# Optimization experiments

Measured on AMD Instinct MI355X. Metric: run time of the kernel, lower is better.

The kernel has to match this reference:

```python
import jax, jax.numpy as jnp
import numpy as np

B, S, D = 8, 1024, 1024   # batch, routed-over rows, feature dim (input_dim)
E = 1024                  # output_dim (== S so gather indices are in range)
K = 2                     # top-k
ALPHA = 0.01


def setup_inputs() -> dict:
    key = jax.random.key(0)
    kx, kw = jax.random.split(key)
    x = jax.random.normal(kx, (B, S, D), dtype=jnp.float32)
    # nn.Linear(input_dim, output_dim, bias=False) weight: [E, D]
    W = jax.random.normal(kw, (E, D), dtype=jnp.float32) / np.sqrt(D).astype(np.float32)
    return {"x": x, "W": W}


def reference(x, W):
    # logits = proj(x): [B, S, E]  (temperature == 1.0 -> no scaling)
    logits = jnp.einsum('bsd,ed->bse', x, W)
    probs = jax.nn.softmax(logits, axis=-1)
    topk_probs, topk_idx = jax.lax.top_k(probs, K)            # [B, S, K]
    # router_selections: gather rows of x along dim 1 -> [B, S, K, D]
    sel = x[jnp.arange(B)[:, None, None], topk_idx]
    # y = sum_k topk_probs * selected rows -> [B, S, D]
    y = jnp.einsum('bsk,bskd->bsd', topk_probs, sel)
    # auxiliary load-balance loss
    router_probs = probs.mean(axis=(0, 1))                    # [E]
    counts = jnp.bincount(topk_idx.reshape(-1), length=E).astype(probs.dtype)
    router_fraction = counts / counts.sum()
    aux_loss = ALPHA * E * jnp.sum(router_probs * router_fraction)
    return y, aux_loss
```

## Files before the change

### kernel.cpp

```cpp
#include <hip/hip_runtime.h>

#define MTOK 8192
#define ED   1024

typedef short s16x8 __attribute__((ext_vector_type(8)));
typedef float f32x4 __attribute__((ext_vector_type(4)));
typedef int   i32x4 __attribute__((ext_vector_type(4)));
typedef unsigned short u16x4 __attribute__((ext_vector_type(4)));

__device__ __forceinline__ unsigned short f2bf(float f) {
    unsigned u = __builtin_bit_cast(unsigned, f);
    u += 0x7fff + ((u >> 16) & 1);
    return (unsigned short)(u >> 16);
}
__device__ __forceinline__ float bf2f(unsigned short h) {
    unsigned u = ((unsigned)h) << 16;
    return __builtin_bit_cast(float, u);
}

__global__ __launch_bounds__(256) void split_bf16_kernel(
        const float* __restrict__ src, unsigned short* __restrict__ hi,
        unsigned short* __restrict__ lo, int n4) {
    int idx = blockIdx.x * 256 + threadIdx.x;
    const int stride = gridDim.x * 256;
    for (; idx < n4; idx += stride) {
        float4 v = ((const float4*)src)[idx];
        u16x4 h, l;
        h[0] = f2bf(v.x); l[0] = f2bf(v.x - bf2f(h[0]));
        h[1] = f2bf(v.y); l[1] = f2bf(v.y - bf2f(h[1]));
        h[2] = f2bf(v.z); l[2] = f2bf(v.z - bf2f(h[2]));
        h[3] = f2bf(v.w); l[3] = f2bf(v.w - bf2f(h[3]));
        ((u16x4*)hi)[idx] = h;
        ((u16x4*)lo)[idx] = l;
    }
}

__device__ __forceinline__ void gload16(const void* g, void* l) {
    __builtin_amdgcn_global_load_lds(
        (const __attribute__((address_space(1))) void*)g,
        (__attribute__((address_space(3))) void*)l, 16, 0, 0);
}

__device__ __forceinline__ int cvtpk(float a, float b) {
    int r;
    asm("v_cvt_pk_bf16_f32 %0, %1, %2" : "=v"(r) : "v"(a), "v"(b));
    return r;
}

__device__ __forceinline__ void cvt_write(void* dstHi, void* dstLo,
                                          const float4 f0, const float4 f1) {
    i32x4 h, l;
    h[0] = cvtpk(f0.x, f0.y); h[1] = cvtpk(f0.z, f0.w);
    h[2] = cvtpk(f1.x, f1.y); h[3] = cvtpk(f1.z, f1.w);
    l[0] = cvtpk(f0.x - __builtin_bit_cast(float, h[0] << 16),
                 f0.y - __builtin_bit_cast(float, h[0] & 0xffff0000));
    l[1] = cvtpk(f0.z - __builtin_bit_cast(float, h[1] << 16),
                 f0.w - __builtin_bit_cast(float, h[1] & 0xffff0000));
    l[2] = cvtpk(f1.x - __builtin_bit_cast(float, h[2] << 16),
                 f1.y - __builtin_bit_cast(float, h[2] & 0xffff0000));
    l[3] = cvtpk(f1.z - __builtin_bit_cast(float, h[3] << 16),
                 f1.w - __builtin_bit_cast(float, h[3] & 0xffff0000));
    *(i32x4*)dstHi = h;
    *(i32x4*)dstLo = l;
}

__global__ __launch_bounds__(256, 2) void gemm_mfma_split_kernel(
        const float* __restrict__ Xf,
        const unsigned short* __restrict__ Whi, const unsigned short* __restrict__ Wlo,
        float* __restrict__ C) {
    __shared__ __align__(16) unsigned char smem[2 * 32768];

    const int bid = blockIdx.x;
    const int xcd = bid & 7;
    const int j   = bid >> 3;
    const int bm  = xcd * 8 + (j >> 3);
    const int bn  = j & 7;

    const int tid  = threadIdx.x;
    const int lane = tid & 63;
    const int wid  = tid >> 6;

    const int srow = lane >> 2;
    const int sg   = (lane & 3) ^ ((lane >> 3) & 3);
    const float* gA = Xf + (size_t)(bm * 128 + wid * 32 + srow) * ED + sg * 8;
    const unsigned short* gB = ((wid < 2) ? Whi : Wlo)
            + (size_t)(bn * 128 + (wid & 1) * 64 + srow) * ED + sg * 8;
    unsigned char* const dB = smem + 16384 + ((wid < 2) ? 0 : 8192) + (wid & 1) * 4096;

    float4 fA0, fA1, fA2, fA3;

#define ALOAD(kk)                                                    \
    fA0 = *(const float4*)(gA + (kk));                               \
    fA1 = *(const float4*)(gA + (kk) + 4);                           \
    fA2 = *(const float4*)(gA + (kk) + 16 * 1024);                   \
    fA3 = *(const float4*)(gA + (kk) + 16 * 1024 + 4);

#define BSTAGE(buf, kk)                                              \
    _Pragma("unroll")                                                \
    for (int c = 0; c < 4; ++c)                                      \
        gload16(gB + (kk) + c * (16 * ED), dB + (buf) * 32768 + c * 1024);

#define AWRITE(buf)                                                              \
    cvt_write(smem + (buf) * 32768 + (2 * wid) * 1024 + lane * 16,               \
              smem + (buf) * 32768 + 8192 + (2 * wid) * 1024 + lane * 16,        \
              fA0, fA1);                                                         \
    cvt_write(smem + (buf) * 32768 + (2 * wid + 1) * 1024 + lane * 16,           \
              smem + (buf) * 32768 + 8192 + (2 * wid + 1) * 1024 + lane * 16,    \
              fA2, fA3);

    const int wm = wid >> 1, wn = wid & 1;
    const int fr = lane & 15, fg = lane >> 4;
    const int pg = fg ^ ((fr >> 1) & 3);
    const int aoff = (wm * 64 + fr) * 32 + pg * 8;
    const int boff = (wn * 64 + fr) * 32 + pg * 8;

    f32x4 acc[4][4] = {};

    ALOAD(0);
    BSTAGE(0, 0);
    AWRITE(0);
    asm volatile("s_waitcnt vmcnt(0) lgkmcnt(0)" ::: "memory");
    __builtin_amdgcn_s_barrier();

    for (int t = 0; t < 32; ++t) {
        const int cur = t & 1;
        if (t < 31) { ALOAD((t + 1) * 32); BSTAGE(cur ^ 1, (t + 1) * 32); }

        const unsigned short* Ah = (const unsigned short*)(smem + cur * 32768);
        const unsigned short* Al = Ah + 4096;
        const unsigned short* Bh = Ah + 8192;
        const unsigned short* Bl = Ah + 12288;

        s16x8 ah[4], al[4], bh[4], bl[4];
#pragma unroll
        for (int i = 0; i < 4; ++i) {
            ah[i] = *(const s16x8*)&Ah[aoff + i * 512];
            al[i] = *(const s16x8*)&Al[aoff + i * 512];
            bh[i] = *(const s16x8*)&Bh[boff + i * 512];
            bl[i] = *(const s16x8*)&Bl[boff + i * 512];
        }
#pragma unroll
        for (int i = 0; i < 4; ++i)
#pragma unroll
            for (int jj = 0; jj < 4; ++jj) {
                acc[i][jj] = __builtin_amdgcn_mfma_f32_16x16x32_bf16(ah[i], bh[jj], acc[i][jj], 0, 0, 0);
                acc[i][jj] = __builtin_amdgcn_mfma_f32_16x16x32_bf16(ah[i], bl[jj], acc[i][jj], 0, 0, 0);
                acc[i][jj] = __builtin_amdgcn_mfma_f32_16x16x32_bf16(al[i], bh[jj], acc[i][jj], 0, 0, 0);
            }

        if (t < 31) AWRITE(cur ^ 1);

        asm volatile("s_waitcnt vmcnt(0) lgkmcnt(0)" ::: "memory");
        __builtin_amdgcn_s_barrier();
    }
#undef ALOAD
#undef BSTAGE
#undef AWRITE

    const int crow = bm * 128 + wm * 64 + fg * 4;
    const int ccol = bn * 128 + wn * 64 + fr;
#pragma unroll
    for (int i = 0; i < 4; ++i)
#pragma unroll
        for (int jj = 0; jj < 4; ++jj)
#pragma unroll
            for (int r = 0; r < 4; ++r)
                C[(size_t)(crow + i * 16 + r) * ED + ccol + jj * 16] = acc[i][jj][r];
}

#define BM 128
#define BN 128
#define BK 32
#define LDA (BM + 4)
#define LDB (BN + 4)

__global__ __launch_bounds__(256) void gemm_logits_kernel(const float* __restrict__ X,
                                                          const float* __restrict__ W,
                                                          float* __restrict__ C) {
    __shared__ float As[BK][LDA];
    __shared__ float Bs[BK][LDB];
    const int bm  = blockIdx.y * BM;
    const int bn  = blockIdx.x * BN;
    const int tid = threadIdx.x;
    const int tx  = tid & 15;
    const int ty  = tid >> 4;
    const int lr  = tid >> 3;
    const int lc  = (tid & 7) << 2;

    float acc[8][8];
#pragma unroll
    for (int i = 0; i < 8; ++i)
#pragma unroll
        for (int j = 0; j < 8; ++j) acc[i][j] = 0.f;

    for (int k0 = 0; k0 < ED; k0 += BK) {
#pragma unroll
        for (int i = 0; i < 4; ++i) {
            const int r = lr + i * 32;
            float4 va = *(const float4*)&X[(size_t)(bm + r) * ED + k0 + lc];
            As[lc + 0][r] = va.x; As[lc + 1][r] = va.y;
            As[lc + 2][r] = va.z; As[lc + 3][r] = va.w;
            float4 vb = *(const float4*)&W[(size_t)(bn + r) * ED + k0 + lc];
            Bs[lc + 0][r] = vb.x; Bs[lc + 1][r] = vb.y;
            Bs[lc + 2][r] = vb.z; Bs[lc + 3][r] = vb.w;
        }
        __syncthreads();
#pragma unroll
        for (int kk = 0; kk < BK; ++kk) {
            float a[8], b[8];
            *(float4*)&a[0] = *(const float4*)&As[kk][ty * 8];
            *(float4*)&a[4] = *(const float4*)&As[kk][ty * 8 + 4];
            *(float4*)&b[0] = *(const float4*)&Bs[kk][tx * 8];
            *(float4*)&b[4] = *(const float4*)&Bs[kk][tx * 8 + 4];
#pragma unroll
            for (int i = 0; i < 8; ++i)
#pragma unroll
                for (int j = 0; j < 8; ++j)
                    acc[i][j] = fmaf(a[i], b[j], acc[i][j]);
        }
        __syncthreads();
    }
#pragma unroll
    for (int i = 0; i < 8; ++i) {
        const int r = bm + ty * 8 + i;
        float4* dst = (float4*)&C[(size_t)r * ED + bn + tx * 8];
        dst[0] = make_float4(acc[i][0], acc[i][1], acc[i][2], acc[i][3]);
        dst[1] = make_float4(acc[i][4], acc[i][5], acc[i][6], acc[i][7]);
    }
}

__device__ __forceinline__ bool better(float v, int i, float bv, int bi) {
    return (v > bv) || (v == bv && i < bi);
}

__global__ __launch_bounds__(256, 8) void softmax_wave_kernel(
        const float* __restrict__ X, float* __restrict__ OUT,
        float* __restrict__ partial, int* __restrict__ counts) {
    __shared__ float L[4 * 1024];
    const int tid  = threadIdx.x;
    const int lane = tid & 63;
    const int w    = tid >> 6;
    const int t    = blockIdx.x * 4 + w;

    const float4* row4 = (const float4*)&OUT[(size_t)t * ED];
    float4 p[4];
#pragma unroll
    for (int i = 0; i < 4; ++i) p[i] = row4[lane + 64 * i];

    float v1 = -1e30f, v2 = -1e30f; int i1 = 0x7fffffff, i2 = 0x7fffffff;
#pragma unroll
    for (int i = 0; i < 4; ++i) {
        const float vv[4] = {p[i].x, p[i].y, p[i].z, p[i].w};
#pragma unroll
        for (int c = 0; c < 4; ++c) {
            const int e = 256 * i + 4 * lane + c;
            const float v = vv[c];
            if (better(v, e, v1, i1)) { v2 = v1; i2 = i1; v1 = v; i1 = e; }
            else if (better(v, e, v2, i2)) { v2 = v; i2 = e; }
        }
    }
#pragma unroll
    for (int off = 32; off; off >>= 1) {
        const float ov1 = __shfl_xor(v1, off); const int oi1 = __shfl_xor(i1, off);
        const float ov2 = __shfl_xor(v2, off); const int oi2 = __shfl_xor(i2, off);
        if (better(ov1, oi1, v1, i1)) {
            float nv2; int ni2;
            if (better(v1, i1, ov2, oi2)) { nv2 = v1; ni2 = i1; }
            else { nv2 = ov2; ni2 = oi2; }
            v1 = ov1; i1 = oi1; v2 = nv2; i2 = ni2;
        } else if (better(ov1, oi1, v2, i2)) { v2 = ov1; i2 = oi1; }
    }
    const float m = v1;

    float s = 0.f;
#pragma unroll
    for (int i = 0; i < 4; ++i) {
        p[i].x = __expf(p[i].x - m); p[i].y = __expf(p[i].y - m);
        p[i].z = __expf(p[i].z - m); p[i].w = __expf(p[i].w - m);
        s += p[i].x + p[i].y + p[i].z + p[i].w;
    }
#pragma unroll
    for (int off = 32; off; off >>= 1) s += __shfl_xor(s, off);
    const float inv = 1.f / s;

#pragma unroll
    for (int i = 0; i < 4; ++i) {
        float4 q = make_float4(p[i].x * inv, p[i].y * inv, p[i].z * inv, p[i].w * inv);
        *(float4*)&L[w * 1024 + i * 256 + lane * 4] = q;
    }

    const float p1 = inv;
    const float p2 = __expf(v2 - m) * inv;
    const int b = t >> 10;
    const float4* x1 = (const float4*)&X[((size_t)(b << 10) + i1) * ED];
    const float4* x2 = (const float4*)&X[((size_t)(b << 10) + i2) * ED];
    float4* yrow = (float4*)&OUT[(size_t)t * ED];
#pragma unroll
    for (int i = 0; i < 4; ++i) {
        const int idx = lane + 64 * i;
        const float4 a = x1[idx];
        const float4 c = x2[idx];
        float4 r;
        r.x = fmaf(p1, a.x, p2 * c.x);
        r.y = fmaf(p1, a.y, p2 * c.y);
        r.z = fmaf(p1, a.z, p2 * c.z);
        r.w = fmaf(p1, a.w, p2 * c.w);
        yrow[idx] = r;
    }

    if (lane == 0) { atomicAdd(&counts[i1], 1); atomicAdd(&counts[i2], 1); }

    __syncthreads();
    float4 s0 = *(float4*)&L[0 * 1024 + tid * 4];
    float4 s1 = *(float4*)&L[1 * 1024 + tid * 4];
    float4 s2 = *(float4*)&L[2 * 1024 + tid * 4];
    float4 s3 = *(float4*)&L[3 * 1024 + tid * 4];
    float4 r;
    r.x = (s0.x + s1.x) + (s2.x + s3.x);
    r.y = (s0.y + s1.y) + (s2.y + s3.y);
    r.z = (s0.z + s1.z) + (s2.z + s3.z);
    r.w = (s0.w + s1.w) + (s2.w + s3.w);
    *(float4*)&partial[(size_t)blockIdx.x * 1024 + tid * 4] = r;
}

__global__ __launch_bounds__(256) void aux1_kernel(const float* __restrict__ partial,
                                                   const int* __restrict__ counts,
                                                   float* __restrict__ dotPartial) {
    __shared__ float red[16][16];
    const int tid = threadIdx.x;
    const int el  = tid & 15;
    const int ch  = tid >> 4;
    const int e   = blockIdx.x * 16 + el;
    float s = 0.f;
    for (int k = 0; k < 128; ++k)
        s += partial[(size_t)(ch * 128 + k) * 1024 + e];
    red[ch][el] = s;
    __syncthreads();
    if (tid < 16) {
        float rs = 0.f;
#pragma unroll
        for (int c = 0; c < 16; ++c) rs += red[c][tid];
        float val = rs * (float)counts[blockIdx.x * 16 + tid];
#pragma unroll
        for (int off = 8; off; off >>= 1) val += __shfl_xor(val, off);
        if (tid == 0) dotPartial[blockIdx.x] = val;
    }
}

__global__ void aux2_kernel(const float* __restrict__ dotPartial, float* __restrict__ out) {
    const int lane = threadIdx.x;
    float v = dotPartial[lane];
#pragma unroll
    for (int off = 32; off; off >>= 1) v += __shfl_xor(v, off);
    if (lane == 0)
        out[(size_t)MTOK * ED] = v * (0.01f * 1024.f / (8192.f * 16384.f));
}

#define TOKS_PER_BLK 16
__global__ __launch_bounds__(256) void softmax_topk_y_kernel(
        const float* __restrict__ X, float* __restrict__ OUT,
        float* __restrict__ router_sum, int* __restrict__ counts) {
    __shared__ float routerLocal[ED];
    __shared__ float redMax[4];
    __shared__ float redSum[4];
    __shared__ float wV1[4]; __shared__ int wI1[4];
    __shared__ float wV2[4]; __shared__ int wI2[4];

    const int tid  = threadIdx.x;
    const int lane = tid & 63;
    const int wave = tid >> 6;

    for (int e = tid; e < ED; e += 256) routerLocal[e] = 0.f;
    __syncthreads();

    const int t0 = blockIdx.x * TOKS_PER_BLK;
    for (int t = t0; t < t0 + TOKS_PER_BLK; ++t) {
        const float* lrow = &OUT[(size_t)t * ED];
        float l[4];
#pragma unroll
        for (int i = 0; i < 4; ++i) l[i] = lrow[tid + i * 256];

        float m = fmaxf(fmaxf(l[0], l[1]), fmaxf(l[2], l[3]));
#pragma unroll
        for (int off = 32; off; off >>= 1) m = fmaxf(m, __shfl_xor(m, off));
        if (lane == 0) redMax[wave] = m;
        __syncthreads();
        m = fmaxf(fmaxf(redMax[0], redMax[1]), fmaxf(redMax[2], redMax[3]));

        float p[4]; float s = 0.f;
#pragma unroll
        for (int i = 0; i < 4; ++i) { p[i] = expf(l[i] - m); s += p[i]; }
#pragma unroll
        for (int off = 32; off; off >>= 1) s += __shfl_xor(s, off);
        if (lane == 0) redSum[wave] = s;

        float v1 = -1e30f, v2 = -1e30f; int i1 = 0x7fffffff, i2 = 0x7fffffff;
#pragma unroll
        for (int i = 0; i < 4; ++i) {
            const float v = l[i]; const int ix = tid + i * 256;
            if (better(v, ix, v1, i1)) { v2 = v1; i2 = i1; v1 = v; i1 = ix; }
            else if (better(v, ix, v2, i2)) { v2 = v; i2 = ix; }
        }
#pragma unroll
        for (int off = 32; off; off >>= 1) {
            const float ov1 = __shfl_xor(v1, off); const int oi1 = __shfl_xor(i1, off);
            const float ov2 = __shfl_xor(v2, off); const int oi2 = __shfl_xor(i2, off);
            if (better(ov1, oi1, v1, i1)) {
                float nv2; int ni2;
                if (better(v1, i1, ov2, oi2)) { nv2 = v1; ni2 = i1; }
                else { nv2 = ov2; ni2 = oi2; }
                v1 = ov1; i1 = oi1; v2 = nv2; i2 = ni2;
            } else if (better(ov1, oi1, v2, i2)) { v2 = ov1; i2 = oi1; }
        }
        if (lane == 0) { wV1[wave] = v1; wI1[wave] = i1; wV2[wave] = v2; wI2[wave] = i2; }
        __syncthreads();

        v1 = wV1[0]; i1 = wI1[0]; v2 = wV2[0]; i2 = wI2[0];
#pragma unroll
        for (int w = 1; w < 4; ++w) {
            const float ov1 = wV1[w]; const int oi1 = wI1[w];
            const float ov2 = wV2[w]; const int oi2 = wI2[w];
            if (better(ov1, oi1, v1, i1)) {
                float nv2; int ni2;
                if (better(v1, i1, ov2, oi2)) { nv2 = v1; ni2 = i1; }
                else { nv2 = ov2; ni2 = oi2; }
                v1 = ov1; i1 = oi1; v2 = nv2; i2 = ni2;
            } else if (better(ov1, oi1, v2, i2)) { v2 = ov1; i2 = oi1; }
        }
        const float stot = redSum[0] + redSum[1] + redSum[2] + redSum[3];
        const float inv = 1.f / stot;

#pragma unroll
        for (int i = 0; i < 4; ++i) routerLocal[tid + i * 256] += p[i] * inv;

        const float p1 = expf(v1 - m) * inv;
        const float p2 = expf(v2 - m) * inv;

        const int b = t >> 10;
        const float4* x1 = (const float4*)&X[((size_t)(b << 10) + i1) * ED];
        const float4* x2 = (const float4*)&X[((size_t)(b << 10) + i2) * ED];
        float4* yrow = (float4*)&OUT[(size_t)t * ED];
        const float4 a = x1[tid];
        const float4 c = x2[tid];
        float4 r;
        r.x = fmaf(p1, a.x, p2 * c.x);
        r.y = fmaf(p1, a.y, p2 * c.y);
        r.z = fmaf(p1, a.z, p2 * c.z);
        r.w = fmaf(p1, a.w, p2 * c.w);
        yrow[tid] = r;

        if (tid == 0) { atomicAdd(&counts[i1], 1); atomicAdd(&counts[i2], 1); }
        __syncthreads();
    }

    for (int e = tid; e < ED; e += 256) atomicAdd(&router_sum[e], routerLocal[e]);
}

__global__ __launch_bounds__(256) void aux_kernel(const float* __restrict__ router_sum,
                                                  const int* __restrict__ counts,
                                                  float* __restrict__ out) {
    __shared__ float red[4];
    const int tid = threadIdx.x;
    float s = 0.f;
    for (int e = tid; e < ED; e += 256)
        s += (router_sum[e] * (1.f / 8192.f)) * ((float)counts[e] * (1.f / 16384.f));
#pragma unroll
    for (int off = 32; off; off >>= 1) s += __shfl_xor(s, off);
    if ((tid & 63) == 0) red[tid >> 6] = s;
    __syncthreads();
    if (tid == 0) out[(size_t)MTOK * ED] = 0.01f * 1024.f * (red[0] + red[1] + red[2] + red[3]);
}

extern "C" void kernel_launch(void* const* d_in, const int* in_sizes, int n_in,
                              void* d_out, int out_size, void* d_ws, size_t ws_size,
                              hipStream_t stream) {
    const float* X = (const float*)d_in[0];
    const float* W = (const float*)d_in[1];
    float* out = (float*)d_out;

    const size_t WS_NEED = (size_t)ED * ED * 2 * sizeof(unsigned short)
                         + (size_t)2048 * 1024 * sizeof(float)
                         + 64 * sizeof(float) + ED * sizeof(int);

    if (ws_size >= WS_NEED) {
        unsigned short* Whi = (unsigned short*)d_ws;
        unsigned short* Wlo = Whi + (size_t)ED * ED;
        float* partial      = (float*)(Wlo + (size_t)ED * ED);
        float* dotPartial   = partial + (size_t)2048 * 1024;
        int*   counts       = (int*)(dotPartial + 64);

        hipMemsetAsync(counts, 0, ED * sizeof(int), stream);
        split_bf16_kernel<<<512, 256, 0, stream>>>(W, Whi, Wlo, ED * ED / 4);
        gemm_mfma_split_kernel<<<512, 256, 0, stream>>>(X, Whi, Wlo, out);
        softmax_wave_kernel<<<MTOK / 4, 256, 0, stream>>>(X, out, partial, counts);
        aux1_kernel<<<64, 256, 0, stream>>>(partial, counts, dotPartial);
        aux2_kernel<<<1, 64, 0, stream>>>(dotPartial, out);
    } else {
        float* router_sum = (float*)d_ws;
        int*   counts     = (int*)((char*)d_ws + ED * sizeof(float));
        hipMemsetAsync(d_ws, 0, ED * (sizeof(float) + sizeof(int)), stream);
        dim3 ggrid(ED / BN, MTOK / BM);
        gemm_logits_kernel<<<ggrid, 256, 0, stream>>>(X, W, out);
        softmax_topk_y_kernel<<<MTOK / TOKS_PER_BLK, 256, 0, stream>>>(X, out, router_sum, counts);
        aux_kernel<<<1, 256, 0, stream>>>(router_sum, counts, out);
    }
}
```

Baseline: 93.70 us.

## Pre-swizzle W into MFMA fragment layout and load B directly to registers

Replaces the flat hi/lo bf16 split of W with a kernel that writes W already arranged in the per-lane MFMA fragment order. The GEMM then loads B fragments straight from global memory into registers, double-buffered across two unrolled steps, instead of staging them through LDS. This halves the LDS footprint and removes the B LDS reads and the vmcnt waits at the barrier. In exchange, B loads now go to global/L2 without LDS reuse, and each wave does more global traffic and holds more registers.

Result: no change. 93.72 us (+0.0%).

```diff
diff --git a/kernel.cpp b/kernel.cpp
--- a/kernel.cpp
+++ b/kernel.cpp
@@ -7,39 +7,6 @@
 typedef float f32x4 __attribute__((ext_vector_type(4)));
 typedef int   i32x4 __attribute__((ext_vector_type(4)));
 typedef unsigned short u16x4 __attribute__((ext_vector_type(4)));
-
-__device__ __forceinline__ unsigned short f2bf(float f) {
-    unsigned u = __builtin_bit_cast(unsigned, f);
-    u += 0x7fff + ((u >> 16) & 1);
-    return (unsigned short)(u >> 16);
-}
-__device__ __forceinline__ float bf2f(unsigned short h) {
-    unsigned u = ((unsigned)h) << 16;
-    return __builtin_bit_cast(float, u);
-}
-
-__global__ __launch_bounds__(256) void split_bf16_kernel(
-        const float* __restrict__ src, unsigned short* __restrict__ hi,
-        unsigned short* __restrict__ lo, int n4) {
-    int idx = blockIdx.x * 256 + threadIdx.x;
-    const int stride = gridDim.x * 256;
-    for (; idx < n4; idx += stride) {
-        float4 v = ((const float4*)src)[idx];
-        u16x4 h, l;
-        h[0] = f2bf(v.x); l[0] = f2bf(v.x - bf2f(h[0]));
-        h[1] = f2bf(v.y); l[1] = f2bf(v.y - bf2f(h[1]));
-        h[2] = f2bf(v.z); l[2] = f2bf(v.z - bf2f(h[2]));
-        h[3] = f2bf(v.w); l[3] = f2bf(v.w - bf2f(h[3]));
-        ((u16x4*)hi)[idx] = h;
-        ((u16x4*)lo)[idx] = l;
-    }
-}
-
-__device__ __forceinline__ void gload16(const void* g, void* l) {
-    __builtin_amdgcn_global_load_lds(
-        (const __attribute__((address_space(1))) void*)g,
-        (__attribute__((address_space(3))) void*)l, 16, 0, 0);
-}
 
 __device__ __forceinline__ int cvtpk(float a, float b) {
     int r;
@@ -64,11 +31,26 @@
     *(i32x4*)dstLo = l;
 }
 
+__global__ __launch_bounds__(256) void wfrag_kernel(
+        const float* __restrict__ W,
+        unsigned short* __restrict__ Bhi, unsigned short* __restrict__ Blo) {
+    const int task = blockIdx.x * 4 + (threadIdx.x >> 6);
+    const int lane = threadIdx.x & 63;
+    const int rowblk = task >> 5;
+    const int kstep  = task & 31;
+    const float* src = W + (size_t)(rowblk * 16 + (lane & 15)) * ED
+                         + kstep * 32 + (lane >> 4) * 8;
+    const float4 f0 = *(const float4*)src;
+    const float4 f1 = *(const float4*)(src + 4);
+    const size_t o = ((size_t)task * 64 + lane) * 8;
+    cvt_write(&Bhi[o], &Blo[o], f0, f1);
+}
+
 __global__ __launch_bounds__(256, 2) void gemm_mfma_split_kernel(
         const float* __restrict__ Xf,
-        const unsigned short* __restrict__ Whi, const unsigned short* __restrict__ Wlo,
+        const unsigned short* __restrict__ Bhi, const unsigned short* __restrict__ Blo,
         float* __restrict__ C) {
-    __shared__ __align__(16) unsigned char smem[2 * 32768];
+    __shared__ __align__(16) unsigned char smem[2 * 16384];
 
     const int bid = blockIdx.x;
     const int xcd = bid & 7;
@@ -83,79 +65,76 @@
     const int srow = lane >> 2;
     const int sg   = (lane & 3) ^ ((lane >> 3) & 3);
     const float* gA = Xf + (size_t)(bm * 128 + wid * 32 + srow) * ED + sg * 8;
-    const unsigned short* gB = ((wid < 2) ? Whi : Wlo)
-            + (size_t)(bn * 128 + (wid & 1) * 64 + srow) * ED + sg * 8;
-    unsigned char* const dB = smem + 16384 + ((wid < 2) ? 0 : 8192) + (wid & 1) * 4096;
 
     float4 fA0, fA1, fA2, fA3;
-
 #define ALOAD(kk)                                                    \
     fA0 = *(const float4*)(gA + (kk));                               \
     fA1 = *(const float4*)(gA + (kk) + 4);                           \
     fA2 = *(const float4*)(gA + (kk) + 16 * 1024);                   \
     fA3 = *(const float4*)(gA + (kk) + 16 * 1024 + 4);
 
-#define BSTAGE(buf, kk)                                              \
-    _Pragma("unroll")                                                \
-    for (int c = 0; c < 4; ++c)                                      \
-        gload16(gB + (kk) + c * (16 * ED), dB + (buf) * 32768 + c * 1024);
-
-#define AWRITE(buf)                                                              \
-    cvt_write(smem + (buf) * 32768 + (2 * wid) * 1024 + lane * 16,               \
-              smem + (buf) * 32768 + 8192 + (2 * wid) * 1024 + lane * 16,        \
-              fA0, fA1);                                                         \
-    cvt_write(smem + (buf) * 32768 + (2 * wid + 1) * 1024 + lane * 16,           \
-              smem + (buf) * 32768 + 8192 + (2 * wid + 1) * 1024 + lane * 16,    \
-              fA2, fA3);
+#define AWRITE(BOFF)                                                             \
+    cvt_write(smem + (BOFF) + (2 * wid) * 1024 + lane * 16,                      \
+              smem + (BOFF) + 8192 + (2 * wid) * 1024 + lane * 16, fA0, fA1);    \
+    cvt_write(smem + (BOFF) + (2 * wid + 1) * 1024 + lane * 16,                  \
+              smem + (BOFF) + 8192 + (2 * wid + 1) * 1024 + lane * 16, fA2, fA3);
 
     const int wm = wid >> 1, wn = wid & 1;
     const int fr = lane & 15, fg = lane >> 4;
     const int pg = fg ^ ((fr >> 1) & 3);
     const int aoff = (wm * 64 + fr) * 32 + pg * 8;
-    const int boff = (wn * 64 + fr) * 32 + pg * 8;
+
+    const unsigned short* gBh = Bhi + (size_t)(bn * 8 + wn * 4) * 16384 + lane * 8;
+    const unsigned short* gBl = Blo + (size_t)(bn * 8 + wn * 4) * 16384 + lane * 8;
+
+    s16x8 bh0[4], bl0[4], bh1[4], bl1[4];
+#define BLOAD(S, T)                                                  \
+    _Pragma("unroll")                                                \
+    for (int i = 0; i < 4; ++i) {                                    \
+        bh##S[i] = *(const s16x8*)(gBh + i * 16384 + (T) * 512);     \
+        bl##S[i] = *(const s16x8*)(gBl + i * 16384 + (T) * 512);     \
+    }
 
     f32x4 acc[4][4] = {};
 
+#define STEP(T, BUFOFF, S, SN)                                                   \
+    {                                                                            \
+        if ((T) < 31) { ALOAD(((T) + 1) * 32); BLOAD(SN, (T) + 1); }             \
+        const unsigned short* Ah = (const unsigned short*)(smem + (BUFOFF));     \
+        const unsigned short* Al = Ah + 4096;                                    \
+        s16x8 ah[4], al[4];                                                      \
+        _Pragma("unroll")                                                        \
+        for (int i = 0; i < 4; ++i) {                                            \
+            ah[i] = *(const s16x8*)&Ah[aoff + i * 512];                          \
+            al[i] = *(const s16x8*)&Al[aoff + i * 512];                          \
+        }                                                                        \
+        _Pragma("unroll")                                                        \
+        for (int i = 0; i < 4; ++i)                                              \
+            _Pragma("unroll")                                                    \
+            for (int jj = 0; jj < 4; ++jj) {                                     \
+                acc[i][jj] = __builtin_amdgcn_mfma_f32_16x16x32_bf16(ah[i], bh##S[jj], acc[i][jj], 0, 0, 0); \
+                acc[i][jj] = __builtin_amdgcn_mfma_f32_16x16x32_bf16(ah[i], bl##S[jj], acc[i][jj], 0, 0, 0); \
+                acc[i][jj] = __builtin_amdgcn_mfma_f32_16x16x32_bf16(al[i], bh##S[jj], acc[i][jj], 0, 0, 0); \
+            }                                                                    \
+        if ((T) < 31) AWRITE((BUFOFF) ^ 16384);                                  \
+        asm volatile("s_waitcnt lgkmcnt(0)" ::: "memory");                       \
+        __builtin_amdgcn_s_barrier();                                            \
+    }
+
     ALOAD(0);
-    BSTAGE(0, 0);
+    BLOAD(0, 0);
     AWRITE(0);
-    asm volatile("s_waitcnt vmcnt(0) lgkmcnt(0)" ::: "memory");
+    asm volatile("s_waitcnt lgkmcnt(0)" ::: "memory");
     __builtin_amdgcn_s_barrier();
 
-    for (int t = 0; t < 32; ++t) {
-        const int cur = t & 1;
-        if (t < 31) { ALOAD((t + 1) * 32); BSTAGE(cur ^ 1, (t + 1) * 32); }
-
-        const unsigned short* Ah = (const unsigned short*)(smem + cur * 32768);
-        const unsigned short* Al = Ah + 4096;
-        const unsigned short* Bh = Ah + 8192;
-        const unsigned short* Bl = Ah + 12288;
-
-        s16x8 ah[4], al[4], bh[4], bl[4];
-#pragma unroll
-        for (int i = 0; i < 4; ++i) {
-            ah[i] = *(const s16x8*)&Ah[aoff + i * 512];
-            al[i] = *(const s16x8*)&Al[aoff + i * 512];
-            bh[i] = *(const s16x8*)&Bh[boff + i * 512];
-            bl[i] = *(const s16x8*)&Bl[boff + i * 512];
-        }
-#pragma unroll
-        for (int i = 0; i < 4; ++i)
-#pragma unroll
-            for (int jj = 0; jj < 4; ++jj) {
-                acc[i][jj] = __builtin_amdgcn_mfma_f32_16x16x32_bf16(ah[i], bh[jj], acc[i][jj], 0, 0, 0);
-                acc[i][jj] = __builtin_amdgcn_mfma_f32_16x16x32_bf16(ah[i], bl[jj], acc[i][jj], 0, 0, 0);
-                acc[i][jj] = __builtin_amdgcn_mfma_f32_16x16x32_bf16(al[i], bh[jj], acc[i][jj], 0, 0, 0);
-            }
-
-        if (t < 31) AWRITE(cur ^ 1);
-
-        asm volatile("s_waitcnt vmcnt(0) lgkmcnt(0)" ::: "memory");
-        __builtin_amdgcn_s_barrier();
-    }
+    for (int t2 = 0; t2 < 32; t2 += 2) {
+        STEP(t2,     0,     0, 1)
+        STEP(t2 + 1, 16384, 1, 0)
+    }
+#undef STEP
+#undef BLOAD
+#undef AWRITE
 #undef ALOAD
-#undef BSTAGE
-#undef AWRITE
 
     const int crow = bm * 128 + wm * 64 + fg * 4;
     const int ccol = bn * 128 + wn * 64 + fr;
@@ -483,15 +462,15 @@
                          + 64 * sizeof(float) + ED * sizeof(int);
 
     if (ws_size >= WS_NEED) {
-        unsigned short* Whi = (unsigned short*)d_ws;
-        unsigned short* Wlo = Whi + (size_t)ED * ED;
-        float* partial      = (float*)(Wlo + (size_t)ED * ED);
+        unsigned short* Bhi = (unsigned short*)d_ws;
+        unsigned short* Blo = Bhi + (size_t)ED * ED;
+        float* partial      = (float*)(Blo + (size_t)ED * ED);
         float* dotPartial   = partial + (size_t)2048 * 1024;
         int*   counts       = (int*)(dotPartial + 64);
 
         hipMemsetAsync(counts, 0, ED * sizeof(int), stream);
-        split_bf16_kernel<<<512, 256, 0, stream>>>(W, Whi, Wlo, ED * ED / 4);
-        gemm_mfma_split_kernel<<<512, 256, 0, stream>>>(X, Whi, Wlo, out);
+        wfrag_kernel<<<512, 256, 0, stream>>>(W, Bhi, Blo);
+        gemm_mfma_split_kernel<<<512, 256, 0, stream>>>(X, Bhi, Blo, out);
         softmax_wave_kernel<<<MTOK / 4, 256, 0, stream>>>(X, out, partial, counts);
         aux1_kernel<<<64, 256, 0, stream>>>(partial, counts, dotPartial);
         aux2_kernel<<<1, 64, 0, stream>>>(dotPartial, out);
```
